# Kernel optimization log

Hardware: AMD Instinct MI355X
Metric: run time of the kernel (lower is better)

The kernel has to match this reference:

```python
import jax, jax.numpy as jnp
import numpy as np
from jax import lax

K = 3  # dynamic/static conv kernel size
C = 64  # n_feat (hard-coded by Linear(64, ...) in the module)


def leaky(x):
    return jax.nn.leaky_relu(x, 0.1)


def conv2d(x, w, b, pad):
    # x: [B,C,H,W], w: [O,I,kh,kw] (OIHW), b: [O]
    y = lax.conv_general_dilated(x, w, (1, 1), [(pad, pad), (pad, pad)],
                                 dimension_numbers=("NCHW", "OIHW", "NCHW"))
    return y + b.reshape(1, -1, 1, 1)


def rda_conv(x, d, k1, k2, cw, cb):
    # x: [B,C,H,W], d: [B,64]
    b, c, h, w = x.shape
    hid = leaky(d @ k1)                        # [B,64]
    kern = (hid @ k2).reshape(b * c, 1, K, K)  # per-(batch,channel) kernel
    pad = (K - 1) // 2
    # depthwise dynamic conv: groups = b*c
    out = lax.conv_general_dilated(x.reshape(1, b * c, h, w), kern, (1, 1),
                                   [(pad, pad), (pad, pad)],
                                   feature_group_count=b * c,
                                   dimension_numbers=("NCHW", "OIHW", "NCHW"))
    out = leaky(out).reshape(b, c, h, w)
    M = jax.nn.sigmoid(conv2d(x, cw, cb, 0))   # [B,1,H,W] gating map
    return out * M + x


def setup_inputs() -> dict:
    key = jax.random.key(0)
    ks = jax.random.split(key, 14)
    s = 0.05
    inp = {
        "x": jax.random.normal(ks[0], (16, C, 128, 128), jnp.float32),
        "d": jax.random.normal(ks[1], (16, C), jnp.float32),
        # RDA_conv 1: kernel MLP (stored as [in,out]) + 1x1 gating conv
        "da1_k1": jax.random.normal(ks[2], (64, 64), jnp.float32) * s,
        "da1_k2": jax.random.normal(ks[3], (64, 64 * K * K), jnp.float32) * s,
        "da1_cw": jax.random.normal(ks[4], (1, C, 1, 1), jnp.float32) * s,
        "da1_cb": jax.random.normal(ks[5], (1,), jnp.float32) * s,
        # RDA_conv 2
        "da2_k1": jax.random.normal(ks[6], (64, 64), jnp.float32) * s,
        "da2_k2": jax.random.normal(ks[7], (64, 64 * K * K), jnp.float32) * s,
        "da2_cw": jax.random.normal(ks[8], (1, C, 1, 1), jnp.float32) * s,
        "da2_cb": jax.random.normal(ks[9], (1,), jnp.float32) * s,
        # static 3x3 convs
        "conv1_w": jax.random.normal(ks[10], (C, C, K, K), jnp.float32) * s,
        "conv1_b": jax.random.normal(ks[11], (C,), jnp.float32) * s,
        "conv2_w": jax.random.normal(ks[12], (C, C, K, K), jnp.float32) * s,
        "conv2_b": jax.random.normal(ks[13], (C,), jnp.float32) * s,
    }
    return inp


def reference(x, d, da1_k1, da1_k2, da1_cw, da1_cb, da2_k1, da2_k2, da2_cw,
              da2_cb, conv1_w, conv1_b, conv2_w, conv2_b):
    pad = (K - 1) // 2
    out = leaky(rda_conv(x, d, da1_k1, da1_k2, da1_cw, da1_cb))
    out = leaky(conv2d(out, conv1_w, conv1_b, pad))
    out = leaky(rda_conv(out, d, da2_k1, da2_k2, da2_cw, da2_cb))
    out = conv2d(out, conv2_w, conv2_b, pad) + x
    return out
```

## Files before the change

kernel.cpp:

```cpp
#include <hip/hip_runtime.h>
#include <hip/hip_bf16.h>
#include <math.h>

#define B_ 16
#define C_ 64
#define H_ 128
#define W_ 128
#define HW_ (H_*W_)
#define CHW_ (C_*HW_)
#define NTOT_ (B_*CHW_)

typedef __attribute__((ext_vector_type(8))) short short8;
typedef __attribute__((ext_vector_type(4))) float float4v;

__device__ __forceinline__ float leaky(float v) { return v > 0.f ? v : 0.1f * v; }
__device__ __forceinline__ float bs2f(short u) {
    return __uint_as_float(((unsigned)(unsigned short)u) << 16);
}
__device__ __forceinline__ short f2bs(float v) {
    __hip_bfloat16 h = __float2bfloat16(v);
    union { __hip_bfloat16 h; short s; } u; u.h = h; return u.s;
}

__global__ __launch_bounds__(192) void k_dyn(
    const float* __restrict__ d,
    const float* __restrict__ k1a, const float* __restrict__ k2a,
    const float* __restrict__ k1b, const float* __restrict__ k2b,
    float* __restrict__ kernA, float* __restrict__ kernB)
{
    const int which = blockIdx.x / 48;
    const int r     = blockIdx.x % 48;
    const int b     = r / 3;
    const int chunk = r % 3;
    const float* k1 = which ? k1b : k1a;
    const float* k2 = which ? k2b : k2a;
    float* outp = which ? kernB : kernA;

    __shared__ float hid[64];
    const int tid = threadIdx.x;
    if (tid < 64) {
        float s = 0.f;
        #pragma unroll
        for (int i = 0; i < 64; ++i) s = fmaf(d[b*64 + i], k1[i*64 + tid], s);
        hid[tid] = leaky(s);
    }
    __syncthreads();
    const int o = chunk * 192 + tid;
    float s = 0.f;
    #pragma unroll
    for (int j = 0; j < 64; ++j) s = fmaf(hid[j], k2[j*576 + o], s);
    outp[b*576 + (o % 9)*64 + (o / 9)] = s;
}

__global__ void k_prepw(const float* __restrict__ W1, const float* __restrict__ W2,
                        __hip_bfloat16* __restrict__ P1, __hip_bfloat16* __restrict__ P2)
{
    const int s = blockIdx.x;
    const int which = blockIdx.y;
    const float* W = which ? W2 : W1;
    __hip_bfloat16* P = which ? P2 : P1;
    const int t = s >> 1, hf = s & 1;
    for (int idx = threadIdx.x; idx < 2048; idx += 256) {
        const int oc = idx >> 5, kk = idx & 31;
        P[s*2048 + idx] = __float2bfloat16(W[oc*576 + (hf*32 + kk)*9 + t]);
    }
}

__global__ __launch_bounds__(256) void k_pre(const float* __restrict__ X,
                                             const float* __restrict__ cw,
                                             const float* __restrict__ cb,
                                             __hip_bfloat16* __restrict__ Xn,
                                             float* __restrict__ G1)
{
    __shared__ float sT[64][65];
    __shared__ float pG[4][64];
    const int b = blockIdx.y;
    const int p0 = blockIdx.x * 64;
    const int tid = threadIdx.x;
    #pragma unroll
    for (int i = 0; i < 16; ++i) {
        int idx = i*256 + tid;
        int c = idx >> 6, p = idx & 63;
        sT[c][p] = X[(size_t)b*CHW_ + (size_t)c*HW_ + p0 + p];
    }
    __syncthreads();
    #pragma unroll
    for (int i = 0; i < 16; ++i) {
        int idx = i*256 + tid;
        int p = idx >> 6, c = idx & 63;
        Xn[((size_t)b*HW_ + p0 + p)*64 + c] = __float2bfloat16(sT[c][p]);
    }
    const int cg = tid >> 6, p = tid & 63;
    float part = 0.f;
    #pragma unroll
    for (int c = 0; c < 16; ++c) part = fmaf(sT[cg*16 + c][p], cw[cg*16 + c], part);
    pG[cg][p] = part;
    __syncthreads();
    if (tid < 64) {
        float g = pG[0][tid] + pG[1][tid] + pG[2][tid] + pG[3][tid] + cb[0];
        G1[(size_t)b*HW_ + p0 + tid] = 1.f / (1.f + __expf(-g));
    }
}

template<int MODE>
__global__ __launch_bounds__(256) void k_rda_conv(
    const __hip_bfloat16* __restrict__ Xn, const float* __restrict__ kernN,
    const float* __restrict__ G, const __hip_bfloat16* __restrict__ Wpk,
    const float* __restrict__ bias, const float* __restrict__ Xres,
    const float* __restrict__ Gcw, const float* __restrict__ Gcb,
    __hip_bfloat16* __restrict__ OutN, float* __restrict__ OutF,
    float* __restrict__ G2)
{
    __shared__ short sA[20*20*64];
    const int tid = threadIdx.x;
    const int b = blockIdx.y;
    const int h0 = (blockIdx.x >> 3) * 16;
    const int w0 = (blockIdx.x & 7) * 16;
    const int lane = tid & 63;
    const int wv = tid >> 6;

    const short* Xs = (const short*)Xn;
    for (int idx = tid; idx < 3200; idx += 256) {
        const int cc = idx & 7;
        const int w = (idx >> 3) % 20;
        const int r = idx / 160;
        const int gh = h0 - 2 + r;
        const int gw = w0 - 2 + w;
        uint4 v = make_uint4(0, 0, 0, 0);
        if ((unsigned)gh < (unsigned)H_ && (unsigned)gw < (unsigned)W_)
            v = *(const uint4*)(Xs + (((size_t)b*H_ + gh)*W_ + gw)*64 + cc*8);
        *(uint4*)(sA + ((r*20 + w)*64 + ((cc ^ (w & 7)) * 8))) = v;
    }

    float k9[9];
    #pragma unroll
    for (int t = 0; t < 9; ++t) k9[t] = kernN[((size_t)b*9 + t)*64 + lane];

    int loff[8];
    #pragma unroll
    for (int jc = 0; jc < 8; ++jc)
        loff[jc] = (((lane >> 3) ^ jc) << 3) + (lane & 7);

    __syncthreads();

    for (int round = 0; round < 5; ++round) {
        const int r = round*4 + wv;
        const bool active = (r < 18);
        float outv[18];
        if (active) {
            const int gh = h0 - 1 + r;
            if ((unsigned)gh < (unsigned)H_) {
                #pragma unroll
                for (int w = 0; w < 18; ++w) outv[w] = 0.f;
                const float* Gp = G + (size_t)b*HW_ + (size_t)gh*W_ + (w0 - 1);
                const short* r0 = sA + (r*20)*64;
                const short* r1 = r0 + 20*64;
                const short* r2 = r1 + 20*64;
                float c1p = 0.f;
                #pragma unroll
                for (int j = 0; j < 20; ++j) {
                    const int off = j*64 + loff[j & 7];
                    const float c0 = bs2f(r0[off]);
                    const float c1 = bs2f(r1[off]);
                    const float c2 = bs2f(r2[off]);
                    #pragma unroll
                    for (int dw = 0; dw < 3; ++dw) {
                        const int w = j - dw;
                        if (w >= 0 && w < 18)
                            outv[w] = fmaf(c0, k9[dw],
                                      fmaf(c1, k9[3+dw],
                                      fmaf(c2, k9[6+dw], outv[w])));
                    }
                    const int wf = j - 2;
                    if (wf >= 0) {
                        const int gw = w0 - 1 + wf;
                        float val = 0.f;
                        if ((unsigned)gw < (unsigned)W_) {
                            const float m = Gp[wf];
                            val = leaky(leaky(outv[wf]) * m + c1p);
                        }
                        outv[wf] = val;
                    }
                    c1p = c1;
                }
            } else {
                #pragma unroll
                for (int w = 0; w < 18; ++w) outv[w] = 0.f;
            }
        }
        __syncthreads();
        if (active) {
            short* wp = sA + (r*20)*64;
            #pragma unroll
            for (int w = 0; w < 18; ++w)
                wp[w*64 + loff[w & 7]] = f2bs(outv[w]);
        }
        __syncthreads();
    }

    const int l15 = lane & 15;
    const int lq = lane >> 4;

    float4v acc[4][4];
    #pragma unroll
    for (int i = 0; i < 4; ++i)
        #pragma unroll
        for (int j = 0; j < 4; ++j) acc[i][j] = (float4v)0.f;

    const short* Wp = (const short*)Wpk;

    #pragma unroll
    for (int s = 0; s < 18; ++s) {
        const int t = s >> 1, hf = s & 1;
        const int dh = t / 3, dwx = t % 3;
        short8 afr[4], bfr[4];
        #pragma unroll
        for (int mt = 0; mt < 4; ++mt) {
            const int r = wv*4 + mt + dh;
            const int w = l15 + dwx;
            const int chunk = (hf*4 + lq) ^ (w & 7);
            afr[mt] = *(const short8*)(sA + ((r*20 + w)*64 + chunk*8));
        }
        #pragma unroll
        for (int nt = 0; nt < 4; ++nt)
            bfr[nt] = *(const short8*)(Wp + ((size_t)s*2048 + (nt*16 + l15)*32 + lq*8));
        #pragma unroll
        for (int mt = 0; mt < 4; ++mt)
            #pragma unroll
            for (int nt = 0; nt < 4; ++nt)
                acc[mt][nt] = __builtin_amdgcn_mfma_f32_16x16x32_bf16(
                    afr[mt], bfr[nt], acc[mt][nt], 0, 0, 0);
    }

    float bs[4], cwv[4], cbv = 0.f;
    #pragma unroll
    for (int nt = 0; nt < 4; ++nt) bs[nt] = bias[nt*16 + l15];
    if (MODE == 0) {
        #pragma unroll
        for (int nt = 0; nt < 4; ++nt) cwv[nt] = Gcw[nt*16 + l15];
        cbv = Gcb[0];
    }

    #pragma unroll
    for (int mt = 0; mt < 4; ++mt) {
        const int pr = wv*4 + mt;
        if (MODE == 0) {
            float vv[4][4];
            #pragma unroll
            for (int nt = 0; nt < 4; ++nt)
                #pragma unroll
                for (int rg = 0; rg < 4; ++rg)
                    vv[nt][rg] = leaky(acc[mt][nt][rg] + bs[nt]);
            #pragma unroll
            for (int nt = 0; nt < 4; ++nt) {
                const int n = nt*16 + l15;
                #pragma unroll
                for (int rg = 0; rg < 4; ++rg) {
                    const int pw = lq*4 + rg;
                    OutN[(((size_t)b*H_ + h0 + pr)*W_ + w0 + pw)*64 + n] =
                        __float2bfloat16(vv[nt][rg]);
                }
            }
            #pragma unroll
            for (int rg = 0; rg < 4; ++rg) {
                float p = vv[0][rg]*cwv[0] + vv[1][rg]*cwv[1]
                        + vv[2][rg]*cwv[2] + vv[3][rg]*cwv[3];
                p += __shfl_xor(p, 1);
                p += __shfl_xor(p, 2);
                p += __shfl_xor(p, 4);
                p += __shfl_xor(p, 8);
                if (l15 == 0)
                    G2[(size_t)b*HW_ + (size_t)(h0 + pr)*W_ + w0 + lq*4 + rg] =
                        1.f / (1.f + __expf(-(p + cbv)));
            }
        } else {
            #pragma unroll
            for (int nt = 0; nt < 4; ++nt) {
                const int n = nt*16 + l15;
                const size_t base = ((size_t)(b*64 + n)*H_ + h0 + pr)*W_ + w0 + lq*4;
                const float4 xr = *(const float4*)(Xres + base);
                float4 v;
                v.x = acc[mt][nt][0] + bs[nt] + xr.x;
                v.y = acc[mt][nt][1] + bs[nt] + xr.y;
                v.z = acc[mt][nt][2] + bs[nt] + xr.z;
                v.w = acc[mt][nt][3] + bs[nt] + xr.w;
                *(float4*)(OutF + base) = v;
            }
        }
    }
}

extern "C" void kernel_launch(void* const* d_in, const int* in_sizes, int n_in,
                              void* d_out, int out_size, void* d_ws, size_t ws_size,
                              hipStream_t stream)
{
    const float* x       = (const float*)d_in[0];
    const float* d       = (const float*)d_in[1];
    const float* da1_k1  = (const float*)d_in[2];
    const float* da1_k2  = (const float*)d_in[3];
    const float* da1_cw  = (const float*)d_in[4];
    const float* da1_cb  = (const float*)d_in[5];
    const float* da2_k1  = (const float*)d_in[6];
    const float* da2_k2  = (const float*)d_in[7];
    const float* da2_cw  = (const float*)d_in[8];
    const float* da2_cb  = (const float*)d_in[9];
    const float* conv1_w = (const float*)d_in[10];
    const float* conv1_b = (const float*)d_in[11];
    const float* conv2_w = (const float*)d_in[12];
    const float* conv2_b = (const float*)d_in[13];
    float* out = (float*)d_out;

    __hip_bfloat16* bufA = (__hip_bfloat16*)d_ws;
    __hip_bfloat16* bufB = bufA + NTOT_;
    float* kernA = (float*)(bufB + NTOT_);
    float* kernB = kernA + 16*576;
    __hip_bfloat16* wpk1 = (__hip_bfloat16*)(kernB + 16*576);
    __hip_bfloat16* wpk2 = wpk1 + 18*64*32;
    float* G1 = (float*)(wpk2 + 18*64*32);
    float* G2 = G1 + (size_t)B_*HW_;

    k_dyn<<<dim3(96), dim3(192), 0, stream>>>(d, da1_k1, da1_k2, da2_k1, da2_k2,
                                              kernA, kernB);
    k_prepw<<<dim3(18, 2), dim3(256), 0, stream>>>(conv1_w, conv2_w, wpk1, wpk2);
    k_pre<<<dim3(HW_/64, B_), dim3(256), 0, stream>>>(x, da1_cw, da1_cb, bufA, G1);
    k_rda_conv<0><<<dim3(64, B_), dim3(256), 0, stream>>>(
        bufA, kernA, G1, wpk1, conv1_b, nullptr, da2_cw, da2_cb, bufB, nullptr, G2);
    k_rda_conv<1><<<dim3(64, B_), dim3(256), 0, stream>>>(
        bufB, kernB, G2, wpk2, conv2_b, x, nullptr, nullptr, nullptr, out, nullptr);
}
```

Baseline: 259.5 us.

## Merge setup kernels and double conv block to 512 threads with in-register row staging

Folds the dynamic-kernel MLP, weight packing and input transpose/gating into one launch to cut kernel-launch overhead. The fused RDA+conv kernel now uses 8 waves per block. The depthwise phase gives each wave 2-3 contiguous rows and holds the last two rows in packed registers, so only one barrier is needed instead of ten. The MFMA phase gives each wave 2 row tiles instead of 4. This raises parallelism and occupancy within the tile at the cost of uneven row assignment and extra registers for held rows.

Result: slower. 272.9 us (+5.2%).

```diff
diff --git a/kernel.cpp b/kernel.cpp
--- a/kernel.cpp
+++ b/kernel.cpp
@@ -22,88 +22,88 @@
     union { __hip_bfloat16 h; short s; } u; u.h = h; return u.s;
 }
 
-__global__ __launch_bounds__(192) void k_dyn(
+__global__ __launch_bounds__(256) void k_setup(
+    const float* __restrict__ X, const float* __restrict__ cw,
+    const float* __restrict__ cb, __hip_bfloat16* __restrict__ Xn,
+    float* __restrict__ G1,
     const float* __restrict__ d,
     const float* __restrict__ k1a, const float* __restrict__ k2a,
     const float* __restrict__ k1b, const float* __restrict__ k2b,
-    float* __restrict__ kernA, float* __restrict__ kernB)
-{
-    const int which = blockIdx.x / 48;
-    const int r     = blockIdx.x % 48;
-    const int b     = r / 3;
-    const int chunk = r % 3;
-    const float* k1 = which ? k1b : k1a;
-    const float* k2 = which ? k2b : k2a;
-    float* outp = which ? kernB : kernA;
-
-    __shared__ float hid[64];
-    const int tid = threadIdx.x;
-    if (tid < 64) {
-        float s = 0.f;
-        #pragma unroll
-        for (int i = 0; i < 64; ++i) s = fmaf(d[b*64 + i], k1[i*64 + tid], s);
-        hid[tid] = leaky(s);
-    }
-    __syncthreads();
-    const int o = chunk * 192 + tid;
-    float s = 0.f;
-    #pragma unroll
-    for (int j = 0; j < 64; ++j) s = fmaf(hid[j], k2[j*576 + o], s);
-    outp[b*576 + (o % 9)*64 + (o / 9)] = s;
-}
-
-__global__ void k_prepw(const float* __restrict__ W1, const float* __restrict__ W2,
-                        __hip_bfloat16* __restrict__ P1, __hip_bfloat16* __restrict__ P2)
-{
-    const int s = blockIdx.x;
-    const int which = blockIdx.y;
-    const float* W = which ? W2 : W1;
-    __hip_bfloat16* P = which ? P2 : P1;
-    const int t = s >> 1, hf = s & 1;
-    for (int idx = threadIdx.x; idx < 2048; idx += 256) {
-        const int oc = idx >> 5, kk = idx & 31;
-        P[s*2048 + idx] = __float2bfloat16(W[oc*576 + (hf*32 + kk)*9 + t]);
-    }
-}
-
-__global__ __launch_bounds__(256) void k_pre(const float* __restrict__ X,
-                                             const float* __restrict__ cw,
-                                             const float* __restrict__ cb,
-                                             __hip_bfloat16* __restrict__ Xn,
-                                             float* __restrict__ G1)
+    float* __restrict__ kernA, float* __restrict__ kernB,
+    const float* __restrict__ W1, const float* __restrict__ W2,
+    __hip_bfloat16* __restrict__ P1, __hip_bfloat16* __restrict__ P2)
 {
     __shared__ float sT[64][65];
     __shared__ float pG[4][64];
-    const int b = blockIdx.y;
-    const int p0 = blockIdx.x * 64;
+    __shared__ float hid[64];
+    const int bid = blockIdx.x;
     const int tid = threadIdx.x;
-    #pragma unroll
-    for (int i = 0; i < 16; ++i) {
-        int idx = i*256 + tid;
-        int c = idx >> 6, p = idx & 63;
-        sT[c][p] = X[(size_t)b*CHW_ + (size_t)c*HW_ + p0 + p];
-    }
-    __syncthreads();
-    #pragma unroll
-    for (int i = 0; i < 16; ++i) {
-        int idx = i*256 + tid;
-        int p = idx >> 6, c = idx & 63;
-        Xn[((size_t)b*HW_ + p0 + p)*64 + c] = __float2bfloat16(sT[c][p]);
-    }
-    const int cg = tid >> 6, p = tid & 63;
-    float part = 0.f;
-    #pragma unroll
-    for (int c = 0; c < 16; ++c) part = fmaf(sT[cg*16 + c][p], cw[cg*16 + c], part);
-    pG[cg][p] = part;
-    __syncthreads();
-    if (tid < 64) {
-        float g = pG[0][tid] + pG[1][tid] + pG[2][tid] + pG[3][tid] + cb[0];
-        G1[(size_t)b*HW_ + p0 + tid] = 1.f / (1.f + __expf(-g));
+
+    if (bid < 4096) {
+        const int b = bid >> 8;
+        const int p0 = (bid & 255) * 64;
+        #pragma unroll
+        for (int i = 0; i < 16; ++i) {
+            int idx = i*256 + tid;
+            int c = idx >> 6, p = idx & 63;
+            sT[c][p] = X[(size_t)b*CHW_ + (size_t)c*HW_ + p0 + p];
+        }
+        __syncthreads();
+        #pragma unroll
+        for (int i = 0; i < 16; ++i) {
+            int idx = i*256 + tid;
+            int p = idx >> 6, c = idx & 63;
+            Xn[((size_t)b*HW_ + p0 + p)*64 + c] = __float2bfloat16(sT[c][p]);
+        }
+        const int cg = tid >> 6, p = tid & 63;
+        float part = 0.f;
+        #pragma unroll
+        for (int c = 0; c < 16; ++c) part = fmaf(sT[cg*16 + c][p], cw[cg*16 + c], part);
+        pG[cg][p] = part;
+        __syncthreads();
+        if (tid < 64) {
+            float g = pG[0][tid] + pG[1][tid] + pG[2][tid] + pG[3][tid] + cb[0];
+            G1[(size_t)b*HW_ + p0 + tid] = 1.f / (1.f + __expf(-g));
+        }
+    } else if (bid < 4192) {
+        const int r2 = bid - 4096;
+        const int which = r2 / 48;
+        const int rr    = r2 % 48;
+        const int b     = rr / 3;
+        const int chunk = rr % 3;
+        const float* k1 = which ? k1b : k1a;
+        const float* k2 = which ? k2b : k2a;
+        float* outp = which ? kernB : kernA;
+        if (tid < 64) {
+            float s = 0.f;
+            #pragma unroll
+            for (int i = 0; i < 64; ++i) s = fmaf(d[b*64 + i], k1[i*64 + tid], s);
+            hid[tid] = leaky(s);
+        }
+        __syncthreads();
+        if (tid < 192) {
+            const int o = chunk * 192 + tid;
+            float s = 0.f;
+            #pragma unroll
+            for (int j = 0; j < 64; ++j) s = fmaf(hid[j], k2[j*576 + o], s);
+            outp[b*576 + (o % 9)*64 + (o / 9)] = s;
+        }
+    } else {
+        const int p = bid - 4192;
+        const int s = p % 18;
+        const int which = p / 18;
+        const float* W = which ? W2 : W1;
+        __hip_bfloat16* P = which ? P2 : P1;
+        const int t = s >> 1, hf = s & 1;
+        for (int idx = tid; idx < 2048; idx += 256) {
+            const int oc = idx >> 5, kk = idx & 31;
+            P[s*2048 + idx] = __float2bfloat16(W[oc*576 + (hf*32 + kk)*9 + t]);
+        }
     }
 }
 
 template<int MODE>
-__global__ __launch_bounds__(256) void k_rda_conv(
+__global__ __launch_bounds__(512, 4) void k_rda_conv(
     const __hip_bfloat16* __restrict__ Xn, const float* __restrict__ kernN,
     const float* __restrict__ G, const __hip_bfloat16* __restrict__ Wpk,
     const float* __restrict__ bias, const float* __restrict__ Xres,
@@ -111,7 +111,7 @@
     __hip_bfloat16* __restrict__ OutN, float* __restrict__ OutF,
     float* __restrict__ G2)
 {
-    __shared__ short sA[20*20*64];
+    __shared__ __align__(16) short sA[20*20*64];
     const int tid = threadIdx.x;
     const int b = blockIdx.y;
     const int h0 = (blockIdx.x >> 3) * 16;
@@ -120,7 +120,7 @@
     const int wv = tid >> 6;
 
     const short* Xs = (const short*)Xn;
-    for (int idx = tid; idx < 3200; idx += 256) {
+    for (int idx = tid; idx < 3200; idx += 512) {
         const int cc = idx & 7;
         const int w = (idx >> 3) % 20;
         const int r = idx / 160;
@@ -141,69 +141,102 @@
     for (int jc = 0; jc < 8; ++jc)
         loff[jc] = (((lane >> 3) ^ jc) << 3) + (lane & 7);
 
+    auto compute_row = [&](int r, float* outv) {
+        const int gh = h0 - 1 + r;
+        if ((unsigned)gh < (unsigned)H_) {
+            #pragma unroll
+            for (int w = 0; w < 18; ++w) outv[w] = 0.f;
+            const float* Gp = G + (size_t)b*HW_ + (size_t)gh*W_ + (w0 - 1);
+            const short* r0 = sA + (r*20)*64;
+            const short* r1 = r0 + 20*64;
+            const short* r2 = r1 + 20*64;
+            float c1p = 0.f;
+            #pragma unroll
+            for (int j = 0; j < 20; ++j) {
+                const int off = j*64 + loff[j & 7];
+                const float c0 = bs2f(r0[off]);
+                const float c1 = bs2f(r1[off]);
+                const float c2 = bs2f(r2[off]);
+                #pragma unroll
+                for (int dw = 0; dw < 3; ++dw) {
+                    const int w = j - dw;
+                    if (w >= 0 && w < 18)
+                        outv[w] = fmaf(c0, k9[dw],
+                                  fmaf(c1, k9[3+dw],
+                                  fmaf(c2, k9[6+dw], outv[w])));
+                }
+                const int wf = j - 2;
+                if (wf >= 0) {
+                    const int gw = w0 - 1 + wf;
+                    float val = 0.f;
+                    if ((unsigned)gw < (unsigned)W_) {
+                        const float m = Gp[wf];
+                        val = leaky(leaky(outv[wf]) * m + c1p);
+                    }
+                    outv[wf] = val;
+                }
+                c1p = c1;
+            }
+        } else {
+            #pragma unroll
+            for (int w = 0; w < 18; ++w) outv[w] = 0.f;
+        }
+    };
+    auto write_rowf = [&](int r, const float* ov) {
+        short* wp = sA + (r*20)*64;
+        #pragma unroll
+        for (int w = 0; w < 18; ++w)
+            wp[w*64 + loff[w & 7]] = f2bs(ov[w]);
+    };
+
     __syncthreads();
 
-    for (int round = 0; round < 5; ++round) {
-        const int r = round*4 + wv;
-        const bool active = (r < 18);
+    const int s0 = (wv < 2) ? wv*3 : 6 + (wv - 2)*2;
+    const int e  = s0 + ((wv < 2) ? 3 : 2);
+
+    unsigned held0[9], held1[9];
+    {
         float outv[18];
-        if (active) {
-            const int gh = h0 - 1 + r;
-            if ((unsigned)gh < (unsigned)H_) {
-                #pragma unroll
-                for (int w = 0; w < 18; ++w) outv[w] = 0.f;
-                const float* Gp = G + (size_t)b*HW_ + (size_t)gh*W_ + (w0 - 1);
-                const short* r0 = sA + (r*20)*64;
-                const short* r1 = r0 + 20*64;
-                const short* r2 = r1 + 20*64;
-                float c1p = 0.f;
-                #pragma unroll
-                for (int j = 0; j < 20; ++j) {
-                    const int off = j*64 + loff[j & 7];
-                    const float c0 = bs2f(r0[off]);
-                    const float c1 = bs2f(r1[off]);
-                    const float c2 = bs2f(r2[off]);
-                    #pragma unroll
-                    for (int dw = 0; dw < 3; ++dw) {
-                        const int w = j - dw;
-                        if (w >= 0 && w < 18)
-                            outv[w] = fmaf(c0, k9[dw],
-                                      fmaf(c1, k9[3+dw],
-                                      fmaf(c2, k9[6+dw], outv[w])));
-                    }
-                    const int wf = j - 2;
-                    if (wf >= 0) {
-                        const int gw = w0 - 1 + wf;
-                        float val = 0.f;
-                        if ((unsigned)gw < (unsigned)W_) {
-                            const float m = Gp[wf];
-                            val = leaky(leaky(outv[wf]) * m + c1p);
-                        }
-                        outv[wf] = val;
-                    }
-                    c1p = c1;
-                }
-            } else {
-                #pragma unroll
-                for (int w = 0; w < 18; ++w) outv[w] = 0.f;
-            }
-        }
-        __syncthreads();
-        if (active) {
-            short* wp = sA + (r*20)*64;
-            #pragma unroll
-            for (int w = 0; w < 18; ++w)
-                wp[w*64 + loff[w & 7]] = f2bs(outv[w]);
-        }
-        __syncthreads();
-    }
+        compute_row(e - 2, outv);
+        #pragma unroll
+        for (int t = 0; t < 9; ++t)
+            held0[t] = (unsigned)(unsigned short)f2bs(outv[2*t])
+                     | ((unsigned)(unsigned short)f2bs(outv[2*t+1]) << 16);
+        compute_row(e - 1, outv);
+        #pragma unroll
+        for (int t = 0; t < 9; ++t)
+            held1[t] = (unsigned)(unsigned short)f2bs(outv[2*t])
+                     | ((unsigned)(unsigned short)f2bs(outv[2*t+1]) << 16);
+    }
+    __syncthreads();
+
+    for (int r = s0; r < e - 2; ++r) {
+        float outv[18];
+        compute_row(r, outv);
+        write_rowf(r, outv);
+    }
+    {
+        short* wp = sA + ((e - 2)*20)*64;
+        #pragma unroll
+        for (int t = 0; t < 9; ++t) {
+            wp[(2*t)*64   + loff[(2*t) & 7]]   = (short)(held0[t] & 0xffff);
+            wp[(2*t+1)*64 + loff[(2*t+1) & 7]] = (short)(held0[t] >> 16);
+        }
+        wp = sA + ((e - 1)*20)*64;
+        #pragma unroll
+        for (int t = 0; t < 9; ++t) {
+            wp[(2*t)*64   + loff[(2*t) & 7]]   = (short)(held1[t] & 0xffff);
+            wp[(2*t+1)*64 + loff[(2*t+1) & 7]] = (short)(held1[t] >> 16);
+        }
+    }
+    __syncthreads();
 
     const int l15 = lane & 15;
     const int lq = lane >> 4;
 
-    float4v acc[4][4];
-    #pragma unroll
-    for (int i = 0; i < 4; ++i)
+    float4v acc[2][4];
+    #pragma unroll
+    for (int i = 0; i < 2; ++i)
         #pragma unroll
         for (int j = 0; j < 4; ++j) acc[i][j] = (float4v)0.f;
 
@@ -213,10 +246,10 @@
     for (int s = 0; s < 18; ++s) {
         const int t = s >> 1, hf = s & 1;
         const int dh = t / 3, dwx = t % 3;
-        short8 afr[4], bfr[4];
-        #pragma unroll
-        for (int mt = 0; mt < 4; ++mt) {
-            const int r = wv*4 + mt + dh;
+        short8 afr[2], bfr[4];
+        #pragma unroll
+        for (int mt = 0; mt < 2; ++mt) {
+            const int r = wv*2 + mt + dh;
             const int w = l15 + dwx;
             const int chunk = (hf*4 + lq) ^ (w & 7);
             afr[mt] = *(const short8*)(sA + ((r*20 + w)*64 + chunk*8));
@@ -225,7 +258,7 @@
         for (int nt = 0; nt < 4; ++nt)
             bfr[nt] = *(const short8*)(Wp + ((size_t)s*2048 + (nt*16 + l15)*32 + lq*8));
         #pragma unroll
-        for (int mt = 0; mt < 4; ++mt)
+        for (int mt = 0; mt < 2; ++mt)
             #pragma unroll
             for (int nt = 0; nt < 4; ++nt)
                 acc[mt][nt] = __builtin_amdgcn_mfma_f32_16x16x32_bf16(
@@ -242,8 +275,8 @@
     }
 
     #pragma unroll
-    for (int mt = 0; mt < 4; ++mt) {
-        const int pr = wv*4 + mt;
+    for (int mt = 0; mt < 2; ++mt) {
+        const int pr = wv*2 + mt;
         if (MODE == 0) {
             float vv[4][4];
             #pragma unroll
@@ -319,12 +352,12 @@
     float* G1 = (float*)(wpk2 + 18*64*32);
     float* G2 = G1 + (size_t)B_*HW_;
 
-    k_dyn<<<dim3(96), dim3(192), 0, stream>>>(d, da1_k1, da1_k2, da2_k1, da2_k2,
-                                              kernA, kernB);
-    k_prepw<<<dim3(18, 2), dim3(256), 0, stream>>>(conv1_w, conv2_w, wpk1, wpk2);
-    k_pre<<<dim3(HW_/64, B_), dim3(256), 0, stream>>>(x, da1_cw, da1_cb, bufA, G1);
-    k_rda_conv<0><<<dim3(64, B_), dim3(256), 0, stream>>>(
+    k_setup<<<dim3(4228), dim3(256), 0, stream>>>(
+        x, da1_cw, da1_cb, bufA, G1,
+        d, da1_k1, da1_k2, da2_k1, da2_k2, kernA, kernB,
+        conv1_w, conv2_w, wpk1, wpk2);
+    k_rda_conv<0><<<dim3(64, B_), dim3(512), 0, stream>>>(
         bufA, kernA, G1, wpk1, conv1_b, nullptr, da2_cw, da2_cb, bufB, nullptr, G2);
-    k_rda_conv<1><<<dim3(64, B_), dim3(256), 0, stream>>>(
+    k_rda_conv<1><<<dim3(64, B_), dim3(512), 0, stream>>>(
         bufB, kernB, G2, wpk2, conv2_b, x, nullptr, nullptr, nullptr, out, nullptr);
 }
```

## Merge setup kernels and compute depthwise stage directly from global memory

Applied to the files above, without the earlier changes.

Three small prologue kernels (dynamic-kernel MLP, weight packing, NCHW→NHWC transpose with gating) are merged into one launch, dispatched by block index. In the fused RDA conv kernel, the 20x20 halo staging of the input into LDS is removed. The depthwise conv now reads its neighbours straight from global memory into registers, in half-row pieces, and writes only the 18x18 result tile to LDS. This drops the extra barriers and shrinks shared memory, which may raise occupancy. The cost is redundant global loads of overlapping rows, which are more latency-sensitive than the old LDS reads.

Result: slower. 438.0 us (+68.8%).

```diff
diff --git a/kernel.cpp b/kernel.cpp
--- a/kernel.cpp
+++ b/kernel.cpp
@@ -22,83 +22,83 @@
     union { __hip_bfloat16 h; short s; } u; u.h = h; return u.s;
 }
 
-__global__ __launch_bounds__(192) void k_dyn(
+__global__ __launch_bounds__(256) void k_setup(
+    const float* __restrict__ X, const float* __restrict__ cw,
+    const float* __restrict__ cb, __hip_bfloat16* __restrict__ Xn,
+    float* __restrict__ G1,
     const float* __restrict__ d,
     const float* __restrict__ k1a, const float* __restrict__ k2a,
     const float* __restrict__ k1b, const float* __restrict__ k2b,
-    float* __restrict__ kernA, float* __restrict__ kernB)
-{
-    const int which = blockIdx.x / 48;
-    const int r     = blockIdx.x % 48;
-    const int b     = r / 3;
-    const int chunk = r % 3;
-    const float* k1 = which ? k1b : k1a;
-    const float* k2 = which ? k2b : k2a;
-    float* outp = which ? kernB : kernA;
-
-    __shared__ float hid[64];
-    const int tid = threadIdx.x;
-    if (tid < 64) {
-        float s = 0.f;
-        #pragma unroll
-        for (int i = 0; i < 64; ++i) s = fmaf(d[b*64 + i], k1[i*64 + tid], s);
-        hid[tid] = leaky(s);
-    }
-    __syncthreads();
-    const int o = chunk * 192 + tid;
-    float s = 0.f;
-    #pragma unroll
-    for (int j = 0; j < 64; ++j) s = fmaf(hid[j], k2[j*576 + o], s);
-    outp[b*576 + (o % 9)*64 + (o / 9)] = s;
-}
-
-__global__ void k_prepw(const float* __restrict__ W1, const float* __restrict__ W2,
-                        __hip_bfloat16* __restrict__ P1, __hip_bfloat16* __restrict__ P2)
-{
-    const int s = blockIdx.x;
-    const int which = blockIdx.y;
-    const float* W = which ? W2 : W1;
-    __hip_bfloat16* P = which ? P2 : P1;
-    const int t = s >> 1, hf = s & 1;
-    for (int idx = threadIdx.x; idx < 2048; idx += 256) {
-        const int oc = idx >> 5, kk = idx & 31;
-        P[s*2048 + idx] = __float2bfloat16(W[oc*576 + (hf*32 + kk)*9 + t]);
-    }
-}
-
-__global__ __launch_bounds__(256) void k_pre(const float* __restrict__ X,
-                                             const float* __restrict__ cw,
-                                             const float* __restrict__ cb,
-                                             __hip_bfloat16* __restrict__ Xn,
-                                             float* __restrict__ G1)
+    float* __restrict__ kernA, float* __restrict__ kernB,
+    const float* __restrict__ W1, const float* __restrict__ W2,
+    __hip_bfloat16* __restrict__ P1, __hip_bfloat16* __restrict__ P2)
 {
     __shared__ float sT[64][65];
     __shared__ float pG[4][64];
-    const int b = blockIdx.y;
-    const int p0 = blockIdx.x * 64;
+    __shared__ float hid[64];
+    const int bid = blockIdx.x;
     const int tid = threadIdx.x;
-    #pragma unroll
-    for (int i = 0; i < 16; ++i) {
-        int idx = i*256 + tid;
-        int c = idx >> 6, p = idx & 63;
-        sT[c][p] = X[(size_t)b*CHW_ + (size_t)c*HW_ + p0 + p];
-    }
-    __syncthreads();
-    #pragma unroll
-    for (int i = 0; i < 16; ++i) {
-        int idx = i*256 + tid;
-        int p = idx >> 6, c = idx & 63;
-        Xn[((size_t)b*HW_ + p0 + p)*64 + c] = __float2bfloat16(sT[c][p]);
-    }
-    const int cg = tid >> 6, p = tid & 63;
-    float part = 0.f;
-    #pragma unroll
-    for (int c = 0; c < 16; ++c) part = fmaf(sT[cg*16 + c][p], cw[cg*16 + c], part);
-    pG[cg][p] = part;
-    __syncthreads();
-    if (tid < 64) {
-        float g = pG[0][tid] + pG[1][tid] + pG[2][tid] + pG[3][tid] + cb[0];
-        G1[(size_t)b*HW_ + p0 + tid] = 1.f / (1.f + __expf(-g));
+
+    if (bid < 4096) {
+        const int b = bid >> 8;
+        const int p0 = (bid & 255) * 64;
+        #pragma unroll
+        for (int i = 0; i < 16; ++i) {
+            int idx = i*256 + tid;
+            int c = idx >> 6, p = idx & 63;
+            sT[c][p] = X[(size_t)b*CHW_ + (size_t)c*HW_ + p0 + p];
+        }
+        __syncthreads();
+        #pragma unroll
+        for (int i = 0; i < 16; ++i) {
+            int idx = i*256 + tid;
+            int p = idx >> 6, c = idx & 63;
+            Xn[((size_t)b*HW_ + p0 + p)*64 + c] = __float2bfloat16(sT[c][p]);
+        }
+        const int cg = tid >> 6, p = tid & 63;
+        float part = 0.f;
+        #pragma unroll
+        for (int c = 0; c < 16; ++c) part = fmaf(sT[cg*16 + c][p], cw[cg*16 + c], part);
+        pG[cg][p] = part;
+        __syncthreads();
+        if (tid < 64) {
+            float g = pG[0][tid] + pG[1][tid] + pG[2][tid] + pG[3][tid] + cb[0];
+            G1[(size_t)b*HW_ + p0 + tid] = 1.f / (1.f + __expf(-g));
+        }
+    } else if (bid < 4192) {
+        const int r2 = bid - 4096;
+        const int which = r2 / 48;
+        const int rr    = r2 % 48;
+        const int b     = rr / 3;
+        const int chunk = rr % 3;
+        const float* k1 = which ? k1b : k1a;
+        const float* k2 = which ? k2b : k2a;
+        float* outp = which ? kernB : kernA;
+        if (tid < 64) {
+            float s = 0.f;
+            #pragma unroll
+            for (int i = 0; i < 64; ++i) s = fmaf(d[b*64 + i], k1[i*64 + tid], s);
+            hid[tid] = leaky(s);
+        }
+        __syncthreads();
+        if (tid < 192) {
+            const int o = chunk * 192 + tid;
+            float s = 0.f;
+            #pragma unroll
+            for (int j = 0; j < 64; ++j) s = fmaf(hid[j], k2[j*576 + o], s);
+            outp[b*576 + (o % 9)*64 + (o / 9)] = s;
+        }
+    } else {
+        const int p = bid - 4192;
+        const int s = p % 18;
+        const int which = p / 18;
+        const float* W = which ? W2 : W1;
+        __hip_bfloat16* P = which ? P2 : P1;
+        const int t = s >> 1, hf = s & 1;
+        for (int idx = tid; idx < 2048; idx += 256) {
+            const int oc = idx >> 5, kk = idx & 31;
+            P[s*2048 + idx] = __float2bfloat16(W[oc*576 + (hf*32 + kk)*9 + t]);
+        }
     }
 }
 
@@ -111,7 +111,7 @@
     __hip_bfloat16* __restrict__ OutN, float* __restrict__ OutF,
     float* __restrict__ G2)
 {
-    __shared__ short sA[20*20*64];
+    __shared__ __align__(16) short sA[18*18*64];
     const int tid = threadIdx.x;
     const int b = blockIdx.y;
     const int h0 = (blockIdx.x >> 3) * 16;
@@ -119,19 +119,6 @@
     const int lane = tid & 63;
     const int wv = tid >> 6;
 
-    const short* Xs = (const short*)Xn;
-    for (int idx = tid; idx < 3200; idx += 256) {
-        const int cc = idx & 7;
-        const int w = (idx >> 3) % 20;
-        const int r = idx / 160;
-        const int gh = h0 - 2 + r;
-        const int gw = w0 - 2 + w;
-        uint4 v = make_uint4(0, 0, 0, 0);
-        if ((unsigned)gh < (unsigned)H_ && (unsigned)gw < (unsigned)W_)
-            v = *(const uint4*)(Xs + (((size_t)b*H_ + gh)*W_ + gw)*64 + cc*8);
-        *(uint4*)(sA + ((r*20 + w)*64 + ((cc ^ (w & 7)) * 8))) = v;
-    }
-
     float k9[9];
     #pragma unroll
     for (int t = 0; t < 9; ++t) k9[t] = kernN[((size_t)b*9 + t)*64 + lane];
@@ -141,62 +128,63 @@
     for (int jc = 0; jc < 8; ++jc)
         loff[jc] = (((lane >> 3) ^ jc) << 3) + (lane & 7);
 
+    const short* Xs = (const short*)Xn;
+    const short* Xb = Xs + (size_t)b*HW_*64 + lane;
+
+    #pragma unroll 2
+    for (int i = 0; i < 9; ++i) {
+        const int k = wv + 4*i;
+        const int r = k >> 1;
+        const int wst = (k & 1) * 9;
+        const int gh = h0 - 1 + r;
+        float outv[9];
+        if ((unsigned)gh < (unsigned)H_) {
+            #pragma unroll
+            for (int w = 0; w < 9; ++w) outv[w] = 0.f;
+            const bool up = (gh > 0), dn = (gh < H_ - 1);
+            const short* p1 = Xb + (size_t)gh*W_*64;
+            const float* Gp = G + (size_t)b*HW_ + (size_t)gh*W_ + (w0 - 1 + wst);
+            float c1p = 0.f;
+            #pragma unroll
+            for (int j = 0; j < 11; ++j) {
+                const int gw = w0 - 2 + wst + j;
+                float c0 = 0.f, c1 = 0.f, c2 = 0.f;
+                if ((unsigned)gw < (unsigned)W_) {
+                    const int o = gw*64;
+                    c1 = bs2f(p1[o]);
+                    if (up) c0 = bs2f(p1[o - W_*64]);
+                    if (dn) c2 = bs2f(p1[o + W_*64]);
+                }
+                #pragma unroll
+                for (int dw = 0; dw < 3; ++dw) {
+                    const int w = j - dw;
+                    if (w >= 0 && w < 9)
+                        outv[w] = fmaf(c0, k9[dw],
+                                  fmaf(c1, k9[3+dw],
+                                  fmaf(c2, k9[6+dw], outv[w])));
+                }
+                const int wf = j - 2;
+                if (wf >= 0 && wf < 9) {
+                    const int gwf = w0 - 1 + wst + wf;
+                    float val = 0.f;
+                    if ((unsigned)gwf < (unsigned)W_) {
+                        const float m = Gp[wf];
+                        val = leaky(leaky(outv[wf]) * m + c1p);
+                    }
+                    outv[wf] = val;
+                }
+                c1p = c1;
+            }
+        } else {
+            #pragma unroll
+            for (int w = 0; w < 9; ++w) outv[w] = 0.f;
+        }
+        short* wp = sA + ((size_t)r*18 + wst)*64;
+        #pragma unroll
+        for (int w = 0; w < 9; ++w)
+            wp[w*64 + loff[(wst + w) & 7]] = f2bs(outv[w]);
+    }
     __syncthreads();
-
-    for (int round = 0; round < 5; ++round) {
-        const int r = round*4 + wv;
-        const bool active = (r < 18);
-        float outv[18];
-        if (active) {
-            const int gh = h0 - 1 + r;
-            if ((unsigned)gh < (unsigned)H_) {
-                #pragma unroll
-                for (int w = 0; w < 18; ++w) outv[w] = 0.f;
-                const float* Gp = G + (size_t)b*HW_ + (size_t)gh*W_ + (w0 - 1);
-                const short* r0 = sA + (r*20)*64;
-                const short* r1 = r0 + 20*64;
-                const short* r2 = r1 + 20*64;
-                float c1p = 0.f;
-                #pragma unroll
-                for (int j = 0; j < 20; ++j) {
-                    const int off = j*64 + loff[j & 7];
-                    const float c0 = bs2f(r0[off]);
-                    const float c1 = bs2f(r1[off]);
-                    const float c2 = bs2f(r2[off]);
-                    #pragma unroll
-                    for (int dw = 0; dw < 3; ++dw) {
-                        const int w = j - dw;
-                        if (w >= 0 && w < 18)
-                            outv[w] = fmaf(c0, k9[dw],
-                                      fmaf(c1, k9[3+dw],
-                                      fmaf(c2, k9[6+dw], outv[w])));
-                    }
-                    const int wf = j - 2;
-                    if (wf >= 0) {
-                        const int gw = w0 - 1 + wf;
-                        float val = 0.f;
-                        if ((unsigned)gw < (unsigned)W_) {
-                            const float m = Gp[wf];
-                            val = leaky(leaky(outv[wf]) * m + c1p);
-                        }
-                        outv[wf] = val;
-                    }
-                    c1p = c1;
-                }
-            } else {
-                #pragma unroll
-                for (int w = 0; w < 18; ++w) outv[w] = 0.f;
-            }
-        }
-        __syncthreads();
-        if (active) {
-            short* wp = sA + (r*20)*64;
-            #pragma unroll
-            for (int w = 0; w < 18; ++w)
-                wp[w*64 + loff[w & 7]] = f2bs(outv[w]);
-        }
-        __syncthreads();
-    }
 
     const int l15 = lane & 15;
     const int lq = lane >> 4;
@@ -219,7 +207,7 @@
             const int r = wv*4 + mt + dh;
             const int w = l15 + dwx;
             const int chunk = (hf*4 + lq) ^ (w & 7);
-            afr[mt] = *(const short8*)(sA + ((r*20 + w)*64 + chunk*8));
+            afr[mt] = *(const short8*)(sA + ((r*18 + w)*64 + chunk*8));
         }
         #pragma unroll
         for (int nt = 0; nt < 4; ++nt)
@@ -319,10 +307,10 @@
     float* G1 = (float*)(wpk2 + 18*64*32);
     float* G2 = G1 + (size_t)B_*HW_;
 
-    k_dyn<<<dim3(96), dim3(192), 0, stream>>>(d, da1_k1, da1_k2, da2_k1, da2_k2,
-                                              kernA, kernB);
-    k_prepw<<<dim3(18, 2), dim3(256), 0, stream>>>(conv1_w, conv2_w, wpk1, wpk2);
-    k_pre<<<dim3(HW_/64, B_), dim3(256), 0, stream>>>(x, da1_cw, da1_cb, bufA, G1);
+    k_setup<<<dim3(4228), dim3(256), 0, stream>>>(
+        x, da1_cw, da1_cb, bufA, G1,
+        d, da1_k1, da1_k2, da2_k1, da2_k2, kernA, kernB,
+        conv1_w, conv2_w, wpk1, wpk2);
     k_rda_conv<0><<<dim3(64, B_), dim3(256), 0, stream>>>(
         bufA, kernA, G1, wpk1, conv1_b, nullptr, da2_cw, da2_cb, bufB, nullptr, G2);
     k_rda_conv<1><<<dim3(64, B_), dim3(256), 0, stream>>>(
```
